# Performance work log

Hardware: AMD Instinct MI355X
Metric: run time of the kernel (lower is better)

Reference implementation:

```python
import jax, jax.numpy as jnp
import numpy as np

# Instant-NGP 2D hash-grid hyperparameters (hard-coded in the flax module)
L = 16          # levels
T = 1 << 20     # table size per level (power of 2)
F = 2           # features per entry
N_MIN = 16      # coarsest resolution; growth factor b == 2 given N_max = 2**19
HASH_PRIME_Y = 2654435761  # pi2 from Instant-NGP spatial hash

_CORNER_OFFS = np.array([[0, 0], [0, 1], [1, 0], [1, 1]], dtype=np.uint32)  # 2D cell corners


def hashgrid_encode(uv, tables):
    """uv: [N,2] in [0,1]; tables: [L,T,F]. Returns [N, L*F]."""
    offs = jnp.asarray(_CORNER_OFFS)            # [4,2] uint32
    offs_b = offs.astype(bool)
    feats = []
    for l in range(L):
        res = N_MIN * (2 ** l)                  # 16, 32, ..., 2**19 (static)
        pos = uv * res                          # [N,2]
        pf = jnp.floor(pos)
        w = pos - pf                            # [N,2] interpolation weights
        c = pf.astype(jnp.uint32)               # [N,2] cell corner
        corner = c[:, None, :] + offs[None]     # [N,4,2]
        if (res + 1) ** 2 <= T:
            # level fits densely in the table: row-major linear index
            idx = corner[..., 0] + corner[..., 1] * jnp.uint32(res + 1)
        else:
            # spatial hash: xor of coordinate * prime, masked to table size
            idx = corner[..., 0] ^ (corner[..., 1] * jnp.uint32(HASH_PRIME_Y))
            idx = idx & jnp.uint32(T - 1)
        f = tables[l][idx]                      # gather: [N,4,F]
        # bilinear weights per corner: prod_d (off_d ? w_d : 1-w_d)
        cw = jnp.prod(jnp.where(offs_b[None], w[:, None, :], 1.0 - w[:, None, :]), axis=-1)  # [N,4]
        feats.append(jnp.einsum('nc,ncf->nf', cw, f))  # [N,F]
    return jnp.concatenate(feats, axis=-1)      # [N, L*F]


def setup_inputs() -> dict:
    key = jax.random.key(0)
    ks = jax.random.split(key, 8)
    N = 1 << 20
    uv = jax.random.uniform(ks[0], (N, 2), dtype=jnp.float32)
    # Instant-NGP init: uniform in [-1e-4, 1e-4]
    tables = jax.random.uniform(ks[1], (L, T, F), dtype=jnp.float32, minval=-1e-4, maxval=1e-4)
    d_in = L * F  # 32
    lecun = lambda k, fi, fo: jax.random.normal(k, (fi, fo), dtype=jnp.float32) / jnp.sqrt(jnp.float32(fi))
    return {
        'uv': uv,
        'tables': tables,
        'w1': lecun(ks[2], d_in, 128), 'b1': jnp.zeros((128,), jnp.float32),
        'w2': lecun(ks[3], 128, 128),  'b2': jnp.zeros((128,), jnp.float32),
        'w3': lecun(ks[4], 128, 3),    'b3': jnp.zeros((3,), jnp.float32),
    }


def reference(uv, tables, w1, b1, w2, b2, w3, b3):
    x = hashgrid_encode(uv, tables)             # [N, 32]
    x = jax.nn.relu(x @ w1 + b1)                # [N, 128]
    x = jax.nn.relu(x @ w2 + b2)                # [N, 128]
    rgb = jax.nn.sigmoid(x @ w3 + b3)           # [N, 3]
    return rgb
```

## Files before the change

kernel.cpp:

```cpp
#include <hip/hip_runtime.h>


#define T_SIZE  (1u << 20)
#define HASH_Y  2654435761u
#define NLVL    16
#define MAXPTS  (1u << 20)

typedef __bf16 bf16x8 __attribute__((ext_vector_type(8)));
typedef float f32x4 __attribute__((ext_vector_type(4)));
typedef unsigned short u16x8 __attribute__((ext_vector_type(8)));
typedef unsigned short u16x4 __attribute__((ext_vector_type(4)));

__device__ unsigned int g_feat[NLVL * MAXPTS];

static __device__ __forceinline__ unsigned short f2bf(float f) {
    union { float f; unsigned u; } v; v.f = f;
    unsigned u = v.u;
    u += 0x7fffu + ((u >> 16) & 1u);
    return (unsigned short)(u >> 16);
}

static __device__ __forceinline__ f32x4 mfma16(u16x8 a, u16x8 b, f32x4 c) {
    return __builtin_amdgcn_mfma_f32_16x16x32_bf16(
        __builtin_bit_cast(bf16x8, a), __builtin_bit_cast(bf16x8, b), c, 0, 0, 0);
}

__global__ __launch_bounds__(256)
void ngp_encode(const float* __restrict__ uv, const float* __restrict__ tables,
                int npts, int bpl)
{
    const int bid = blockIdx.x;
    const int lvl = bid / bpl;
    const int blk = bid - lvl * bpl;
    const int base = (blk << 10) + (threadIdx.x << 2);
    if (base >= npts) return;

    const unsigned res = 16u << lvl;
    const float fres = (float)res;
    const unsigned rp1 = res + 1u;
    const unsigned mask = T_SIZE - 1u;
    const bool dense = lvl < 6;
    const float2* __restrict__ t2 = (const float2*)tables + (size_t)lvl * T_SIZE;

    const float4* u4 = (const float4*)(uv + (size_t)base * 2);
    float4 ua = u4[0], ub = u4[1];
    float2 pts[4] = { {ua.x, ua.y}, {ua.z, ua.w}, {ub.x, ub.y}, {ub.z, ub.w} };

    unsigned pk[4];
#pragma unroll
    for (int u = 0; u < 4; ++u) {
        float px = pts[u].x * fres, py = pts[u].y * fres;
        float fx = floorf(px), fy = floorf(py);
        float wx = px - fx, wy = py - fy;
        unsigned cx = (unsigned)fx, cy = (unsigned)fy;
        unsigned hy0 = cy * HASH_Y, hy1 = (cy + 1u) * HASH_Y;
        unsigned i00 = dense ? (cx + cy * rp1)              : ((cx ^ hy0) & mask);
        unsigned i01 = dense ? (cx + (cy + 1u) * rp1)       : ((cx ^ hy1) & mask);
        unsigned i10 = dense ? (cx + 1u + cy * rp1)         : (((cx + 1u) ^ hy0) & mask);
        unsigned i11 = dense ? (cx + 1u + (cy + 1u) * rp1)  : (((cx + 1u) ^ hy1) & mask);
        float2 f00 = t2[i00], f01 = t2[i01], f10 = t2[i10], f11 = t2[i11];
        float w00 = (1.f - wx) * (1.f - wy);
        float w01 = (1.f - wx) * wy;
        float w10 = wx * (1.f - wy);
        float w11 = wx * wy;
        float g0 = w00 * f00.x + w01 * f01.x + w10 * f10.x + w11 * f11.x;
        float g1 = w00 * f00.y + w01 * f01.y + w10 * f10.y + w11 * f11.y;
        pk[u] = (unsigned)f2bf(g0) | ((unsigned)f2bf(g1) << 16);
    }
    *(uint4*)(g_feat + (size_t)lvl * npts + base) = make_uint4(pk[0], pk[1], pk[2], pk[3]);
}

__global__ __launch_bounds__(256, 2)
void ngp_mlp(const float* __restrict__ w1, const float* __restrict__ b1,
             const float* __restrict__ w2, const float* __restrict__ b2,
             const float* __restrict__ w3, const float* __restrict__ b3,
             float* __restrict__ out, int npts)
{
    __shared__ __align__(16) unsigned short w2T[128 * 136];
    __shared__ __align__(16) unsigned short hbuf[4 * 16 * 136];
    __shared__ float b1s[128], b2s[128];

    const int tid = threadIdx.x;
    for (int e = tid; e < 128 * 128; e += 256) {
        int i = e >> 7, o = e & 127;
        w2T[o * 136 + i] = f2bf(w2[e]);
    }
    if (tid < 128) { b1s[tid] = b1[tid]; b2s[tid] = b2[tid]; }
    __syncthreads();

    const int lane = tid & 63;
    const int wv = tid >> 6;
    const int lanelo = lane & 15;
    const int quad = lane >> 4;

    u16x8 a1[8];
#pragma unroll
    for (int mt = 0; mt < 8; ++mt)
#pragma unroll
        for (int j = 0; j < 8; ++j)
            a1[mt][j] = f2bf(w1[(quad * 8 + j) * 128 + mt * 16 + lanelo]);

    u16x8 a3[4];
#pragma unroll
    for (int ks = 0; ks < 4; ++ks)
#pragma unroll
        for (int j = 0; j < 8; ++j) {
            int k = ks * 32 + quad * 8 + j;
            a3[ks][j] = (lanelo < 3) ? f2bf(w3[k * 3 + lanelo]) : (unsigned short)0;
        }

    const int NT = npts >> 4;
    const int nwaves = gridDim.x * 4;
    const int gwave = blockIdx.x * 4 + wv;
    const int niter = (NT + nwaves - 1) / nwaves;

    unsigned short* hp = hbuf + (wv * 16 + lanelo) * 136;

    for (int it = 0; it < niter; ++it) {
        int tile = gwave + it * nwaves;
        bool act = tile < NT;
        int pt = (tile << 4) + lanelo;

        if (act) {
            u16x8 xb;
#pragma unroll
            for (int i = 0; i < 4; ++i) {
                unsigned fp = g_feat[(size_t)((quad << 2) + i) * npts + pt];
                xb[2 * i]     = (unsigned short)(fp & 0xffffu);
                xb[2 * i + 1] = (unsigned short)(fp >> 16);
            }
            f32x4 z = {0.f, 0.f, 0.f, 0.f};
            f32x4 d[8];
#pragma unroll
            for (int mt = 0; mt < 8; ++mt) d[mt] = mfma16(a1[mt], xb, z);
#pragma unroll
            for (int mt = 0; mt < 8; ++mt) {
                u16x4 pk;
#pragma unroll
                for (int r = 0; r < 4; ++r) {
                    float hv = d[mt][r] + b1s[mt * 16 + quad * 4 + r];
                    pk[r] = f2bf(fmaxf(hv, 0.f));
                }
                *(u16x4*)(hp + mt * 16 + quad * 4) = pk;
            }
        }
        __syncthreads();
        if (act) {
            f32x4 z = {0.f, 0.f, 0.f, 0.f};
            f32x4 e[8];
#pragma unroll
            for (int mt = 0; mt < 8; ++mt) e[mt] = z;
#pragma unroll
            for (int ks = 0; ks < 4; ++ks) {
                u16x8 bb = *(const u16x8*)(hp + ks * 32 + quad * 8);
#pragma unroll
                for (int mt = 0; mt < 8; ++mt) {
                    u16x8 aa = *(const u16x8*)(w2T + (mt * 16 + lanelo) * 136 + ks * 32 + quad * 8);
                    e[mt] = mfma16(aa, bb, e[mt]);
                }
            }
#pragma unroll
            for (int mt = 0; mt < 8; ++mt) {
                u16x4 pk;
#pragma unroll
                for (int r = 0; r < 4; ++r) {
                    float hv = e[mt][r] + b2s[mt * 16 + quad * 4 + r];
                    pk[r] = f2bf(fmaxf(hv, 0.f));
                }
                *(u16x4*)(hp + mt * 16 + quad * 4) = pk;
            }
        }
        __syncthreads();
        if (act) {
            f32x4 o3 = {0.f, 0.f, 0.f, 0.f};
#pragma unroll
            for (int ks = 0; ks < 4; ++ks) {
                u16x8 bb = *(const u16x8*)(hp + ks * 32 + quad * 8);
                o3 = mfma16(a3[ks], bb, o3);
            }
            if (quad == 0) {
                float* op = out + (size_t)pt * 3;
#pragma unroll
                for (int r = 0; r < 3; ++r) {
                    float lv = o3[r] + b3[r];
                    op[r] = 1.f / (1.f + expf(-lv));
                }
            }
        }
    }
}

extern "C" void kernel_launch(void* const* d_in, const int* in_sizes, int n_in,
                              void* d_out, int out_size, void* d_ws, size_t ws_size,
                              hipStream_t stream) {
    const float* uv     = (const float*)d_in[0];
    const float* tables = (const float*)d_in[1];
    const float* w1     = (const float*)d_in[2];
    const float* b1     = (const float*)d_in[3];
    const float* w2     = (const float*)d_in[4];
    const float* b2     = (const float*)d_in[5];
    const float* w3     = (const float*)d_in[6];
    const float* b3     = (const float*)d_in[7];
    float* out = (float*)d_out;
    int npts = in_sizes[0] / 2;

    int bpl = (npts + 1023) >> 10;
    hipLaunchKernelGGL(ngp_encode, dim3(NLVL * bpl), dim3(256), 0, stream,
                       uv, tables, npts, bpl);

    hipLaunchKernelGGL(ngp_mlp, dim3(2048), dim3(256), 0, stream,
                       w1, b1, w2, b2, w3, b3, out, npts);
}
```

Before: 537.9 us.

## Pack hash tables to bf16, batch encode gathers, prefetch features and drop MLP barriers

A new pre-pass converts the fp32 hash tables into packed bf16 pairs in a device buffer, so each corner gather in the encoder reads 4 bytes instead of 8. The encoder issues all 16 gathers before interpolating, giving more loads in flight. The MLP kernel removes the __syncthreads calls, since each wave only touches its own shared rows, and prefetches the next tile's features into registers. The cost is an extra pass that reads 128MB and writes 64MB on every call, plus bf16 rounding of the table values.

```diff
diff --git a/kernel.cpp b/kernel.cpp
--- a/kernel.cpp
+++ b/kernel.cpp
@@ -11,6 +11,7 @@
 typedef unsigned short u16x8 __attribute__((ext_vector_type(8)));
 typedef unsigned short u16x4 __attribute__((ext_vector_type(4)));
 
+__device__ unsigned int g_tbl[NLVL * T_SIZE];
 __device__ unsigned int g_feat[NLVL * MAXPTS];
 
 static __device__ __forceinline__ unsigned short f2bf(float f) {
@@ -20,14 +21,38 @@
     return (unsigned short)(u >> 16);
 }
 
+static __device__ __forceinline__ unsigned packbf(float a, float b) {
+    return (unsigned)f2bf(a) | ((unsigned)f2bf(b) << 16);
+}
+
+static __device__ __forceinline__ float bflo(unsigned p) {
+    union { unsigned u; float f; } v; v.u = p << 16; return v.f;
+}
+static __device__ __forceinline__ float bfhi(unsigned p) {
+    union { unsigned u; float f; } v; v.u = p & 0xffff0000u; return v.f;
+}
+
 static __device__ __forceinline__ f32x4 mfma16(u16x8 a, u16x8 b, f32x4 c) {
     return __builtin_amdgcn_mfma_f32_16x16x32_bf16(
         __builtin_bit_cast(bf16x8, a), __builtin_bit_cast(bf16x8, b), c, 0, 0, 0);
 }
 
 __global__ __launch_bounds__(256)
-void ngp_encode(const float* __restrict__ uv, const float* __restrict__ tables,
-                int npts, int bpl)
+void ngp_pack(const float* __restrict__ tables)
+{
+    unsigned i = (blockIdx.x * 256u + threadIdx.x) * 4u;
+    const float4* s = (const float4*)(tables + (size_t)i * 2);
+    float4 a = s[0], b = s[1];
+    uint4 o;
+    o.x = packbf(a.x, a.y);
+    o.y = packbf(a.z, a.w);
+    o.z = packbf(b.x, b.y);
+    o.w = packbf(b.z, b.w);
+    *(uint4*)(g_tbl + i) = o;
+}
+
+__global__ __launch_bounds__(256)
+void ngp_encode(const float* __restrict__ uv, int npts, int bpl)
 {
     const int bid = blockIdx.x;
     const int lvl = bid / bpl;
@@ -40,32 +65,45 @@
     const unsigned rp1 = res + 1u;
     const unsigned mask = T_SIZE - 1u;
     const bool dense = lvl < 6;
-    const float2* __restrict__ t2 = (const float2*)tables + (size_t)lvl * T_SIZE;
+    const unsigned* __restrict__ tl = g_tbl + (size_t)lvl * T_SIZE;
 
     const float4* u4 = (const float4*)(uv + (size_t)base * 2);
     float4 ua = u4[0], ub = u4[1];
-    float2 pts[4] = { {ua.x, ua.y}, {ua.z, ua.w}, {ub.x, ub.y}, {ub.z, ub.w} };
-
-    unsigned pk[4];
+    float pxa[4] = {ua.x, ua.z, ub.x, ub.z};
+    float pya[4] = {ua.y, ua.w, ub.y, ub.w};
+
+    unsigned i00[4], i01[4], i10[4], i11[4];
+    float wx[4], wy[4];
 #pragma unroll
     for (int u = 0; u < 4; ++u) {
-        float px = pts[u].x * fres, py = pts[u].y * fres;
+        float px = pxa[u] * fres, py = pya[u] * fres;
         float fx = floorf(px), fy = floorf(py);
-        float wx = px - fx, wy = py - fy;
+        wx[u] = px - fx; wy[u] = py - fy;
         unsigned cx = (unsigned)fx, cy = (unsigned)fy;
         unsigned hy0 = cy * HASH_Y, hy1 = (cy + 1u) * HASH_Y;
-        unsigned i00 = dense ? (cx + cy * rp1)              : ((cx ^ hy0) & mask);
-        unsigned i01 = dense ? (cx + (cy + 1u) * rp1)       : ((cx ^ hy1) & mask);
-        unsigned i10 = dense ? (cx + 1u + cy * rp1)         : (((cx + 1u) ^ hy0) & mask);
-        unsigned i11 = dense ? (cx + 1u + (cy + 1u) * rp1)  : (((cx + 1u) ^ hy1) & mask);
-        float2 f00 = t2[i00], f01 = t2[i01], f10 = t2[i10], f11 = t2[i11];
-        float w00 = (1.f - wx) * (1.f - wy);
-        float w01 = (1.f - wx) * wy;
-        float w10 = wx * (1.f - wy);
-        float w11 = wx * wy;
-        float g0 = w00 * f00.x + w01 * f01.x + w10 * f10.x + w11 * f11.x;
-        float g1 = w00 * f00.y + w01 * f01.y + w10 * f10.y + w11 * f11.y;
-        pk[u] = (unsigned)f2bf(g0) | ((unsigned)f2bf(g1) << 16);
+        i00[u] = dense ? (cx + cy * rp1)              : ((cx ^ hy0) & mask);
+        i01[u] = dense ? (cx + (cy + 1u) * rp1)       : ((cx ^ hy1) & mask);
+        i10[u] = dense ? (cx + 1u + cy * rp1)         : (((cx + 1u) ^ hy0) & mask);
+        i11[u] = dense ? (cx + 1u + (cy + 1u) * rp1)  : (((cx + 1u) ^ hy1) & mask);
+    }
+    unsigned e00[4], e01[4], e10[4], e11[4];
+#pragma unroll
+    for (int u = 0; u < 4; ++u) {
+        e00[u] = tl[i00[u]];
+        e01[u] = tl[i01[u]];
+        e10[u] = tl[i10[u]];
+        e11[u] = tl[i11[u]];
+    }
+    unsigned pk[4];
+#pragma unroll
+    for (int u = 0; u < 4; ++u) {
+        float w00 = (1.f - wx[u]) * (1.f - wy[u]);
+        float w01 = (1.f - wx[u]) * wy[u];
+        float w10 = wx[u] * (1.f - wy[u]);
+        float w11 = wx[u] * wy[u];
+        float g0 = w00 * bflo(e00[u]) + w01 * bflo(e01[u]) + w10 * bflo(e10[u]) + w11 * bflo(e11[u]);
+        float g1 = w00 * bfhi(e00[u]) + w01 * bfhi(e01[u]) + w10 * bfhi(e10[u]) + w11 * bfhi(e11[u]);
+        pk[u] = packbf(g0, g1);
     }
     *(uint4*)(g_feat + (size_t)lvl * npts + base) = make_uint4(pk[0], pk[1], pk[2], pk[3]);
 }
@@ -108,85 +146,95 @@
             int k = ks * 32 + quad * 8 + j;
             a3[ks][j] = (lanelo < 3) ? f2bf(w3[k * 3 + lanelo]) : (unsigned short)0;
         }
+    float b3r0 = b3[0], b3r1 = b3[1], b3r2 = b3[2];
 
     const int NT = npts >> 4;
     const int nwaves = gridDim.x * 4;
     const int gwave = blockIdx.x * 4 + wv;
-    const int niter = (NT + nwaves - 1) / nwaves;
 
     unsigned short* hp = hbuf + (wv * 16 + lanelo) * 136;
-
-    for (int it = 0; it < niter; ++it) {
-        int tile = gwave + it * nwaves;
-        bool act = tile < NT;
+    const int lvlbase = quad << 2;
+
+    unsigned c0 = 0, c1 = 0, c2 = 0, c3 = 0;
+    if (gwave < NT) {
+        int pt = (gwave << 4) + lanelo;
+        c0 = g_feat[(size_t)(lvlbase + 0) * npts + pt];
+        c1 = g_feat[(size_t)(lvlbase + 1) * npts + pt];
+        c2 = g_feat[(size_t)(lvlbase + 2) * npts + pt];
+        c3 = g_feat[(size_t)(lvlbase + 3) * npts + pt];
+    }
+
+    for (int tile = gwave; tile < NT; tile += nwaves) {
         int pt = (tile << 4) + lanelo;
 
-        if (act) {
-            u16x8 xb;
-#pragma unroll
-            for (int i = 0; i < 4; ++i) {
-                unsigned fp = g_feat[(size_t)((quad << 2) + i) * npts + pt];
-                xb[2 * i]     = (unsigned short)(fp & 0xffffu);
-                xb[2 * i + 1] = (unsigned short)(fp >> 16);
+        u16x8 xb;
+        xb[0] = (unsigned short)(c0 & 0xffffu); xb[1] = (unsigned short)(c0 >> 16);
+        xb[2] = (unsigned short)(c1 & 0xffffu); xb[3] = (unsigned short)(c1 >> 16);
+        xb[4] = (unsigned short)(c2 & 0xffffu); xb[5] = (unsigned short)(c2 >> 16);
+        xb[6] = (unsigned short)(c3 & 0xffffu); xb[7] = (unsigned short)(c3 >> 16);
+
+        int tn = tile + nwaves;
+        unsigned n0 = 0, n1 = 0, n2 = 0, n3 = 0;
+        if (tn < NT) {
+            int ptn = (tn << 4) + lanelo;
+            n0 = g_feat[(size_t)(lvlbase + 0) * npts + ptn];
+            n1 = g_feat[(size_t)(lvlbase + 1) * npts + ptn];
+            n2 = g_feat[(size_t)(lvlbase + 2) * npts + ptn];
+            n3 = g_feat[(size_t)(lvlbase + 3) * npts + ptn];
+        }
+
+        f32x4 z = {0.f, 0.f, 0.f, 0.f};
+        f32x4 d[8];
+#pragma unroll
+        for (int mt = 0; mt < 8; ++mt) d[mt] = mfma16(a1[mt], xb, z);
+#pragma unroll
+        for (int mt = 0; mt < 8; ++mt) {
+            u16x4 pk;
+#pragma unroll
+            for (int r = 0; r < 4; ++r) {
+                float hv = d[mt][r] + b1s[mt * 16 + quad * 4 + r];
+                pk[r] = f2bf(fmaxf(hv, 0.f));
             }
-            f32x4 z = {0.f, 0.f, 0.f, 0.f};
-            f32x4 d[8];
-#pragma unroll
-            for (int mt = 0; mt < 8; ++mt) d[mt] = mfma16(a1[mt], xb, z);
+            *(u16x4*)(hp + mt * 16 + quad * 4) = pk;
+        }
+
+        f32x4 e[8];
+#pragma unroll
+        for (int mt = 0; mt < 8; ++mt) e[mt] = z;
+#pragma unroll
+        for (int ks = 0; ks < 4; ++ks) {
+            u16x8 bb = *(const u16x8*)(hp + ks * 32 + quad * 8);
 #pragma unroll
             for (int mt = 0; mt < 8; ++mt) {
-                u16x4 pk;
-#pragma unroll
-                for (int r = 0; r < 4; ++r) {
-                    float hv = d[mt][r] + b1s[mt * 16 + quad * 4 + r];
-                    pk[r] = f2bf(fmaxf(hv, 0.f));
-                }
-                *(u16x4*)(hp + mt * 16 + quad * 4) = pk;
+                u16x8 aa = *(const u16x8*)(w2T + (mt * 16 + lanelo) * 136 + ks * 32 + quad * 8);
+                e[mt] = mfma16(aa, bb, e[mt]);
             }
         }
-        __syncthreads();
-        if (act) {
-            f32x4 z = {0.f, 0.f, 0.f, 0.f};
-            f32x4 e[8];
-#pragma unroll
-            for (int mt = 0; mt < 8; ++mt) e[mt] = z;
-#pragma unroll
-            for (int ks = 0; ks < 4; ++ks) {
-                u16x8 bb = *(const u16x8*)(hp + ks * 32 + quad * 8);
-#pragma unroll
-                for (int mt = 0; mt < 8; ++mt) {
-                    u16x8 aa = *(const u16x8*)(w2T + (mt * 16 + lanelo) * 136 + ks * 32 + quad * 8);
-                    e[mt] = mfma16(aa, bb, e[mt]);
-                }
+#pragma unroll
+        for (int mt = 0; mt < 8; ++mt) {
+            u16x4 pk;
+#pragma unroll
+            for (int r = 0; r < 4; ++r) {
+                float hv = e[mt][r] + b2s[mt * 16 + quad * 4 + r];
+                pk[r] = f2bf(fmaxf(hv, 0.f));
             }
-#pragma unroll
-            for (int mt = 0; mt < 8; ++mt) {
-                u16x4 pk;
-#pragma unroll
-                for (int r = 0; r < 4; ++r) {
-                    float hv = e[mt][r] + b2s[mt * 16 + quad * 4 + r];
-                    pk[r] = f2bf(fmaxf(hv, 0.f));
-                }
-                *(u16x4*)(hp + mt * 16 + quad * 4) = pk;
-            }
-        }
-        __syncthreads();
-        if (act) {
-            f32x4 o3 = {0.f, 0.f, 0.f, 0.f};
-#pragma unroll
-            for (int ks = 0; ks < 4; ++ks) {
-                u16x8 bb = *(const u16x8*)(hp + ks * 32 + quad * 8);
-                o3 = mfma16(a3[ks], bb, o3);
-            }
-            if (quad == 0) {
-                float* op = out + (size_t)pt * 3;
-#pragma unroll
-                for (int r = 0; r < 3; ++r) {
-                    float lv = o3[r] + b3[r];
-                    op[r] = 1.f / (1.f + expf(-lv));
-                }
-            }
-        }
+            *(u16x4*)(hp + mt * 16 + quad * 4) = pk;
+        }
+
+        f32x4 o3 = {0.f, 0.f, 0.f, 0.f};
+#pragma unroll
+        for (int ks = 0; ks < 4; ++ks) {
+            u16x8 bb = *(const u16x8*)(hp + ks * 32 + quad * 8);
+            o3 = mfma16(a3[ks], bb, o3);
+        }
+        if (quad == 0) {
+            float* op = out + (size_t)pt * 3;
+            op[0] = 1.f / (1.f + expf(-(o3[0] + b3r0)));
+            op[1] = 1.f / (1.f + expf(-(o3[1] + b3r1)));
+            op[2] = 1.f / (1.f + expf(-(o3[2] + b3r2)));
+        }
+
+        c0 = n0; c1 = n1; c2 = n2; c3 = n3;
     }
 }
 
@@ -204,9 +252,12 @@
     float* out = (float*)d_out;
     int npts = in_sizes[0] / 2;
 
+    hipLaunchKernelGGL(ngp_pack, dim3((NLVL * T_SIZE) / 1024), dim3(256), 0, stream,
+                       tables);
+
     int bpl = (npts + 1023) >> 10;
     hipLaunchKernelGGL(ngp_encode, dim3(NLVL * bpl), dim3(256), 0, stream,
-                       uv, tables, npts, bpl);
+                       uv, npts, bpl);
 
     hipLaunchKernelGGL(ngp_mlp, dim3(2048), dim3(256), 0, stream,
                        w1, b1, w2, b2, w3, b3, out, npts);
```

Measured after the change: 676.6 us. +25.8%, slower.
